# Performance work log

Hardware: AMD Instinct MI355X
Metric: run time of the kernel (lower is better)

## Reference

```python
import jax, jax.numpy as jnp
import numpy as np

T, NB, NCLASS, L = 256, 64, 7357, 50


def setup_inputs() -> dict:
    key = jax.random.key(0)
    k1, k2 = jax.random.split(key)
    dense_pred = jax.random.normal(k1, (T, NB, NCLASS), dtype=jnp.float32)
    target = jax.random.randint(k2, (NB, L), 0, NCLASS, dtype=jnp.int64)
    return {"dense_pred": dense_pred, "target": target}


def reference(dense_pred, target):
    # dense_pred: [T, nB, nClass], target: [nB, L] int labels, 0 = stop/blank
    nB, Llen = target.shape
    nClass = dense_pred.shape[-1]
    dense_prob = jax.nn.softmax(dense_pred, axis=2)  # [T, nB, nClass]

    # The torch loop zeroes hollow_param[tt[j]] for j until the FIRST 0 in the
    # target sequence (break). valid[b, j] == 1 iff target[b, :j+1] are all nonzero.
    valid = jnp.cumprod((target != 0).astype(jnp.int32), axis=1)  # [nB, L]
    # Invalid positions map to class 0, which is zeroed unconditionally anyway.
    eff_idx = jnp.where(valid == 1, target, 0)  # [nB, L]

    hollow = jnp.ones((nB, nClass), dtype=dense_pred.dtype)
    hollow = hollow.at[:, 0].set(0.0)
    rows = jnp.broadcast_to(jnp.arange(nB)[:, None], (nB, Llen))
    hollow = hollow.at[rows, eff_idx].set(0.0)  # scatter zeros at target classes

    prob_sum = dense_prob.sum(0)  # [nB, nClass]
    whace_loss = (prob_sum * hollow).mean()
    return whace_loss
```

## Files before the change

### kernel.cpp

```cpp
#include <hip/hip_runtime.h>
#include <math.h>

#define TT 256
#define NB 64
#define NC 7357
#define LL 50
#define NROWS (TT * NB)

__global__ void prep_kernel(const int* __restrict__ target,
                            int* __restrict__ nz, int* __restrict__ cls) {
    int b = threadIdx.x;
    if (b >= NB) return;
    int list[LL + 1];
    int n = 0;
    list[n++] = 0;
    for (int j = 0; j < LL; ++j) {
        int t = target[b * LL + j];
        if (t == 0) break;
        bool found = false;
        for (int k = 0; k < n; ++k) {
            if (list[k] == t) { found = true; break; }
        }
        if (!found) list[n++] = t;
    }
    nz[b] = n;
    for (int k = 0; k < n; ++k) cls[b * 64 + k] = list[k];
}

__global__ __launch_bounds__(256) void row_kernel(const float* __restrict__ x,
                                                  const int* __restrict__ nz,
                                                  const int* __restrict__ cls,
                                                  float* __restrict__ partial) {
    const int row = blockIdx.x;
    const int b = row & (NB - 1);
    const int tid = threadIdx.x;
    const float* rp = x + (size_t)row * NC;
    const float C = 1.4426950408889634f;

    const int peel = (4 - (row & 3)) & 3;
    const int rem = NC - peel;
    const int nvec = rem >> 2;
    const int tail = rem & 3;
    const float4* vp = (const float4*)(rp + peel);

    float xg = -INFINITY;
    const int n = nz[b];
    if (tid < n) xg = rp[cls[b * 64 + tid]];

    float ex1 = -INFINITY, ex2 = -INFINITY;
    if (tid < peel) ex1 = rp[tid];
    if (tid < tail) ex2 = rp[peel + (nvec << 2) + tid];

    float4 q0 = vp[tid];
    float4 q1 = vp[tid + 256];
    float4 q2 = vp[tid + 512];
    float4 q3 = vp[tid + 768];
    float s = exp2f(q0.x * C) + exp2f(q0.y * C) + exp2f(q0.z * C) + exp2f(q0.w * C);
    s += exp2f(q1.x * C) + exp2f(q1.y * C) + exp2f(q1.z * C) + exp2f(q1.w * C);
    s += exp2f(q2.x * C) + exp2f(q2.y * C) + exp2f(q2.z * C) + exp2f(q2.w * C);
    s += exp2f(q3.x * C) + exp2f(q3.y * C) + exp2f(q3.z * C) + exp2f(q3.w * C);

    float4 q4 = vp[tid + 1024];
    float4 q5 = vp[tid + 1280];
    float4 q6 = vp[tid + 1536];
    float4 q7 = make_float4(-INFINITY, -INFINITY, -INFINITY, -INFINITY);
    const int v7 = tid + 1792;
    if (v7 < nvec) q7 = vp[v7];
    s += exp2f(q4.x * C) + exp2f(q4.y * C) + exp2f(q4.z * C) + exp2f(q4.w * C);
    s += exp2f(q5.x * C) + exp2f(q5.y * C) + exp2f(q5.z * C) + exp2f(q5.w * C);
    s += exp2f(q6.x * C) + exp2f(q6.y * C) + exp2f(q6.z * C) + exp2f(q6.w * C);
    s += exp2f(q7.x * C) + exp2f(q7.y * C) + exp2f(q7.z * C) + exp2f(q7.w * C);

    s += exp2f(ex1 * C) + exp2f(ex2 * C);
    float z = exp2f(xg * C);

    for (int o = 32; o > 0; o >>= 1) {
        s += __shfl_down(s, o);
        z += __shfl_down(z, o);
    }
    __shared__ float ssum[4];
    __shared__ float zsum[4];
    const int wave = tid >> 6;
    if ((tid & 63) == 0) { ssum[wave] = s; zsum[wave] = z; }
    __syncthreads();
    if (tid == 0) {
        float S = ssum[0] + ssum[1] + ssum[2] + ssum[3];
        float Z = zsum[0] + zsum[1] + zsum[2] + zsum[3];
        partial[row] = 1.0f - Z / S;
    }
}

__global__ __launch_bounds__(256) void final_kernel(const float* __restrict__ partial,
                                                    float* __restrict__ out) {
    float s = 0.0f;
    for (int i = threadIdx.x; i < NROWS; i += 256) s += partial[i];
    for (int o = 32; o > 0; o >>= 1) s += __shfl_down(s, o);
    __shared__ float sr[4];
    const int wave = threadIdx.x >> 6;
    if ((threadIdx.x & 63) == 0) sr[wave] = s;
    __syncthreads();
    if (threadIdx.x == 0)
        out[0] = (sr[0] + sr[1] + sr[2] + sr[3]) * (1.0f / ((float)NB * (float)NC));
}

extern "C" void kernel_launch(void* const* d_in, const int* in_sizes, int n_in,
                              void* d_out, int out_size, void* d_ws, size_t ws_size,
                              hipStream_t stream) {
    const float* dense_pred = (const float*)d_in[0];
    const int* target = (const int*)d_in[1];
    float* out = (float*)d_out;

    int* nz = (int*)d_ws;
    int* cls = nz + 64;
    float* partial = (float*)(cls + 64 * 64);

    prep_kernel<<<1, 64, 0, stream>>>(target, nz, cls);
    row_kernel<<<NROWS, 256, 0, stream>>>(dense_pred, nz, cls, partial);
    final_kernel<<<1, 256, 0, stream>>>(partial, out);
}
```

Baseline: 218.5 us.

## Process each row with a single wave, two rows per wave, dropping block sync

Changes the work split so each 64-lane wave reduces a whole softmax row by itself, handling two rows in sequence, instead of a 256-thread block per row. This removes the shared-memory reduction and __syncthreads, and cuts the grid from 16384 to 2048 blocks. In exchange, each wave issues fewer loads in flight per row and runs a longer serial loop, which may reduce memory-level parallelism for a bandwidth-bound kernel.

Measured after the change: 226.6 us. 3.7% more time.

```diff
diff --git a/kernel.cpp b/kernel.cpp
--- a/kernel.cpp
+++ b/kernel.cpp
@@ -6,6 +6,8 @@
 #define NC 7357
 #define LL 50
 #define NROWS (TT * NB)
+#define NBLK 2048
+#define ROWS_PER_WAVE 2
 
 __global__ void prep_kernel(const int* __restrict__ target,
                             int* __restrict__ nz, int* __restrict__ cls) {
@@ -31,62 +33,55 @@
                                                   const int* __restrict__ nz,
                                                   const int* __restrict__ cls,
                                                   float* __restrict__ partial) {
-    const int row = blockIdx.x;
-    const int b = row & (NB - 1);
-    const int tid = threadIdx.x;
-    const float* rp = x + (size_t)row * NC;
+    const int lane = threadIdx.x & 63;
+    const int gwave = (blockIdx.x << 2) | (threadIdx.x >> 6);
     const float C = 1.4426950408889634f;
 
-    const int peel = (4 - (row & 3)) & 3;
-    const int rem = NC - peel;
-    const int nvec = rem >> 2;
-    const int tail = rem & 3;
-    const float4* vp = (const float4*)(rp + peel);
+#pragma unroll
+    for (int r = 0; r < ROWS_PER_WAVE; ++r) {
+        const int row = gwave * ROWS_PER_WAVE + r;
+        const int b = row & (NB - 1);
+        const float* rp = x + (size_t)row * NC;
 
-    float xg = -INFINITY;
-    const int n = nz[b];
-    if (tid < n) xg = rp[cls[b * 64 + tid]];
+        const int peel = (4 - (row & 3)) & 3;
+        const int rem = NC - peel;
+        const int nvec = rem >> 2;
+        const int tail = rem & 3;
+        const float4* vp = (const float4*)(rp + peel);
 
-    float ex1 = -INFINITY, ex2 = -INFINITY;
-    if (tid < peel) ex1 = rp[tid];
-    if (tid < tail) ex2 = rp[peel + (nvec << 2) + tid];
+        const int n = nz[b];
+        float xg = (lane < n) ? rp[cls[b * 64 + lane]] : -INFINITY;
 
-    float4 q0 = vp[tid];
-    float4 q1 = vp[tid + 256];
-    float4 q2 = vp[tid + 512];
-    float4 q3 = vp[tid + 768];
-    float s = exp2f(q0.x * C) + exp2f(q0.y * C) + exp2f(q0.z * C) + exp2f(q0.w * C);
-    s += exp2f(q1.x * C) + exp2f(q1.y * C) + exp2f(q1.z * C) + exp2f(q1.w * C);
-    s += exp2f(q2.x * C) + exp2f(q2.y * C) + exp2f(q2.z * C) + exp2f(q2.w * C);
-    s += exp2f(q3.x * C) + exp2f(q3.y * C) + exp2f(q3.z * C) + exp2f(q3.w * C);
+        float ex1 = (lane < peel) ? rp[lane] : -INFINITY;
+        float ex2 = (lane < tail) ? rp[peel + (nvec << 2) + lane] : -INFINITY;
 
-    float4 q4 = vp[tid + 1024];
-    float4 q5 = vp[tid + 1280];
-    float4 q6 = vp[tid + 1536];
-    float4 q7 = make_float4(-INFINITY, -INFINITY, -INFINITY, -INFINITY);
-    const int v7 = tid + 1792;
-    if (v7 < nvec) q7 = vp[v7];
-    s += exp2f(q4.x * C) + exp2f(q4.y * C) + exp2f(q4.z * C) + exp2f(q4.w * C);
-    s += exp2f(q5.x * C) + exp2f(q5.y * C) + exp2f(q5.z * C) + exp2f(q5.w * C);
-    s += exp2f(q6.x * C) + exp2f(q6.y * C) + exp2f(q6.z * C) + exp2f(q6.w * C);
-    s += exp2f(q7.x * C) + exp2f(q7.y * C) + exp2f(q7.z * C) + exp2f(q7.w * C);
+        float s = exp2f(ex1 * C) + exp2f(ex2 * C);
 
-    s += exp2f(ex1 * C) + exp2f(ex2 * C);
-    float z = exp2f(xg * C);
+        int i = lane;
+#pragma unroll
+        for (int c = 0; c < 7; ++c) {
+            float4 q0 = vp[i];
+            float4 q1 = vp[i + 64];
+            float4 q2 = vp[i + 128];
+            float4 q3 = vp[i + 192];
+            s += exp2f(q0.x * C) + exp2f(q0.y * C) + exp2f(q0.z * C) + exp2f(q0.w * C);
+            s += exp2f(q1.x * C) + exp2f(q1.y * C) + exp2f(q1.z * C) + exp2f(q1.w * C);
+            s += exp2f(q2.x * C) + exp2f(q2.y * C) + exp2f(q2.z * C) + exp2f(q2.w * C);
+            s += exp2f(q3.x * C) + exp2f(q3.y * C) + exp2f(q3.z * C) + exp2f(q3.w * C);
+            i += 256;
+        }
+        if (i < nvec) {
+            float4 q = vp[i];
+            s += exp2f(q.x * C) + exp2f(q.y * C) + exp2f(q.z * C) + exp2f(q.w * C);
+        }
 
-    for (int o = 32; o > 0; o >>= 1) {
-        s += __shfl_down(s, o);
-        z += __shfl_down(z, o);
-    }
-    __shared__ float ssum[4];
-    __shared__ float zsum[4];
-    const int wave = tid >> 6;
-    if ((tid & 63) == 0) { ssum[wave] = s; zsum[wave] = z; }
-    __syncthreads();
-    if (tid == 0) {
-        float S = ssum[0] + ssum[1] + ssum[2] + ssum[3];
-        float Z = zsum[0] + zsum[1] + zsum[2] + zsum[3];
-        partial[row] = 1.0f - Z / S;
+        float z = exp2f(xg * C);
+
+        for (int o = 32; o > 0; o >>= 1) {
+            s += __shfl_down(s, o);
+            z += __shfl_down(z, o);
+        }
+        if (lane == 0) partial[row] = 1.0f - z / s;
     }
 }
 
@@ -115,6 +110,6 @@
     float* partial = (float*)(cls + 64 * 64);
 
     prep_kernel<<<1, 64, 0, stream>>>(target, nz, cls);
-    row_kernel<<<NROWS, 256, 0, stream>>>(dense_pred, nz, cls, partial);
+    row_kernel<<<NBLK, 256, 0, stream>>>(dense_pred, nz, cls, partial);
     final_kernel<<<1, 256, 0, stream>>>(partial, out);
 }
```
